# Optimization experiments

Hardware: AMD Instinct MI355X
Metric: run time of the kernel (lower is better)

Reference implementation:

```python
import jax, jax.numpy as jnp
import numpy as np

EPS = 1e-10


def _log_scaling(feats):
    """Raw feats (..., 15): xmin,ymin,xmax,ymax,area,angle,pca_big,pca_small,hu1..hu7
    -> (..., 17): xmin..area, log|pca_big..hu7|, lshape, cosangle, sinangle."""
    lshape = jnp.sqrt(feats[..., 7:8]) / (jnp.sqrt(feats[..., 6:7]) + EPS)
    cosangle = jnp.cos(feats[..., 5:6])
    sinangle = jnp.sin(feats[..., 5:6])
    logged = jnp.log(jnp.abs(feats[..., 5:]) + EPS)  # cols 5..14 logged
    # original drops the (logged) angle column 5 and keeps logged cols 6..14
    return jnp.concatenate([feats[..., :5], logged[..., 1:], lshape, cosangle, sinangle], axis=-1)


def _make_parents(n_trees, P, seed=0):
    """Valid topologically-ordered tree: parent[p] < p, parent[0] = 0 (root)."""
    rng = np.random.default_rng(seed)
    idx = np.arange(P)
    high = np.maximum(idx, 1)
    par = rng.integers(0, 2**31 - 1, size=(n_trees, P)) % high[None, :]
    par[:, 0] = 0
    return par.astype(np.int32)


def setup_inputs() -> dict:
    key = jax.random.key(0)
    k1, k2, k3, k4 = jax.random.split(key, 4)
    B, N, H, W = 2, 2, 1024, 1024
    P = H * W
    x = jax.random.normal(k1, (B, N, H, W), dtype=jnp.float32) * 10.0
    weight = jax.random.uniform(k2, (N, 17, 1), dtype=jnp.float32, minval=-0.01, maxval=0.01)
    bias = jnp.zeros((N, 1), dtype=jnp.float32)
    attrs = jax.random.uniform(k3, (B, N, P, 15), dtype=jnp.float32) * 4.0
    parents = jnp.asarray(_make_parents(B * N, P).reshape(B, N, P))
    return {"x": x, "weight": weight, "bias": bias, "attrs": attrs, "parents": parents}


def _path_sum(contrib_pad, par_pad, P):
    """Pointer-doubling root-to-node path sums over a tree with sentinel at index P."""
    iters = max(int(np.ceil(np.log2(max(P, 2)))), 1)

    def body(i, carry):
        v, p = carry
        return v + v[p], p[p]

    v, _ = jax.lax.fori_loop(0, iters, body, (contrib_pad, par_pad))
    return v[:P]


def reference(x, weight, bias, attrs, parents):
    B, N, H, W = x.shape
    P = H * W
    xf = x.reshape(B, N, P)
    idx = jnp.arange(P, dtype=parents.dtype)
    is_root = parents == idx  # (B,N,P)
    parent_vals = jnp.take_along_axis(xf, parents, axis=-1)
    diff = jnp.where(is_root, xf, xf - parent_vals)  # per-node gray-level increment
    feats = _log_scaling(attrs)  # (B,N,P,17)
    lin = jnp.einsum('bnpf,nfo->bnpo', feats, weight) + bias[None, :, None, :]
    scores = jax.nn.sigmoid(lin[..., 0])  # (B,N,P)
    contrib = diff * scores
    # sentinel node P with contribution 0; roots point at the sentinel
    sent = jnp.full((B, N, 1), P, dtype=parents.dtype)
    par_pad = jnp.concatenate([jnp.where(is_root, P, parents), sent], axis=-1)
    contrib_pad = jnp.concatenate([contrib, jnp.zeros((B, N, 1), x.dtype)], axis=-1)
    out = jax.vmap(jax.vmap(lambda c, p: _path_sum(c, p, P)))(contrib_pad, par_pad)
    return out.reshape(B, N, H, W)
```

## Files before the change

### kernel.cpp

```cpp
#include <hip/hip_runtime.h>
#include <math.h>

#define EPSF 1e-10f
#define P_NODES (1 << 20)
#define T_FRONT 65536
#define T_MID   262144

struct __align__(8) NodePair {
    float v;
    int   par;
};

__global__ __launch_bounds__(256) void score_kernel(
    const float* __restrict__ x,
    const float* __restrict__ weight,
    const float* __restrict__ bias,
    const float* __restrict__ attrs,
    const int*   __restrict__ parents,
    NodePair*    __restrict__ dst,
    int N)
{
    __shared__ float sA[256 * 15];

    const int t = threadIdx.x;
    const int blockBase = blockIdx.x * 256;
    const int idx = blockBase + t;

    const float4* ab4 = (const float4*)(attrs + (size_t)blockBase * 15);
    float4* sA4 = (float4*)sA;
#pragma unroll
    for (int k = t; k < 960; k += 256)
        sA4[k] = ab4[k];

    const int tree = blockBase >> 20;
    const int n    = tree % N;
    const float* w = weight + n * 17;
    const float  b = bias[n];

    __syncthreads();

    const float* a = &sA[t * 15];

    float acc = b;
    acc += a[0] * w[0];
    acc += a[1] * w[1];
    acc += a[2] * w[2];
    acc += a[3] * w[3];
    acc += a[4] * w[4];

    const float a5 = a[5];
    const float a6 = a[6];
    const float a7 = a[7];

    acc += __logf(fabsf(a6)    + EPSF) * w[5];
    acc += __logf(fabsf(a7)    + EPSF) * w[6];
    acc += __logf(fabsf(a[8])  + EPSF) * w[7];
    acc += __logf(fabsf(a[9])  + EPSF) * w[8];
    acc += __logf(fabsf(a[10]) + EPSF) * w[9];
    acc += __logf(fabsf(a[11]) + EPSF) * w[10];
    acc += __logf(fabsf(a[12]) + EPSF) * w[11];
    acc += __logf(fabsf(a[13]) + EPSF) * w[12];
    acc += __logf(fabsf(a[14]) + EPSF) * w[13];

    const float lshape = __fsqrt_rn(a7) / (__fsqrt_rn(a6) + EPSF);
    acc += lshape * w[14];
    acc += __cosf(a5) * w[15];
    acc += __sinf(a5) * w[16];

    const float score = 1.0f / (1.0f + __expf(-acc));

    const int   p   = idx & (P_NODES - 1);
    const int   par = parents[idx];
    const float xv  = x[idx];

    NodePair r;
    if (par == p) {
        r.v   = xv * score;
        r.par = -1;
    } else {
        r.v   = (xv - x[(idx - p) + par]) * score;
        r.par = par;
    }
    dst[idx] = r;
}

__global__ __launch_bounds__(256) void frontier_kernel(
    const NodePair* __restrict__ pairs,
    float*          __restrict__ out)
{
    const int j  = blockIdx.x * blockDim.x + threadIdx.x;
    const int p0 = j * 2;
    if (p0 >= T_FRONT) return;

    const int base = blockIdx.y << 20;
    const NodePair* tp = pairs + base;

    float4 r = *(const float4*)(tp + p0);
    float s0 = r.x;  int c0 = __float_as_int(r.y);
    float s1 = r.z;  int c1 = __float_as_int(r.w);

    while (c0 >= 0 || c1 >= 0) {
        NodePair q0, q1;
        bool a0 = (c0 >= 0), a1 = (c1 >= 0);
        if (a0) q0 = tp[c0];
        if (a1) q1 = tp[c1];
        if (a0) { s0 += q0.v; c0 = q0.par; }
        if (a1) { s1 += q1.v; c1 = q1.par; }
    }

    float2 o; o.x = s0; o.y = s1;
    *(float2*)(out + base + p0) = o;
}

__global__ __launch_bounds__(256) void chunk_kernel(
    const NodePair* __restrict__ pairs,
    float*          __restrict__ out,
    int lo, int hi)
{
    const int j  = blockIdx.x * blockDim.x + threadIdx.x;
    const int p0 = lo + j * 2;
    if (p0 >= hi) return;

    const int base = blockIdx.y << 20;
    const NodePair* tp = pairs + base;

    float4 r = *(const float4*)(tp + p0);
    float s0 = r.x;  int c0 = __float_as_int(r.y);
    float s1 = r.z;  int c1 = __float_as_int(r.w);

    bool a0 = (c0 >= lo), a1 = (c1 >= lo);
    while (a0 || a1) {
        NodePair q0, q1;
        if (a0) q0 = tp[c0];
        if (a1) q1 = tp[c1];
        if (a0) { s0 += q0.v; c0 = q0.par; a0 = (c0 >= lo); }
        if (a1) { s1 += q1.v; c1 = q1.par; a1 = (c1 >= lo); }
    }
    s0 += out[base + c0];
    s1 += out[base + c1];

    float2 o; o.x = s0; o.y = s1;
    *(float2*)(out + base + p0) = o;
}

extern "C" void kernel_launch(void* const* d_in, const int* in_sizes, int n_in,
                              void* d_out, int out_size, void* d_ws, size_t ws_size,
                              hipStream_t stream)
{
    const float* x       = (const float*)d_in[0];
    const float* weight  = (const float*)d_in[1];
    const float* bias    = (const float*)d_in[2];
    const float* attrs   = (const float*)d_in[3];
    const int*   parents = (const int*)d_in[4];
    float*       out     = (float*)d_out;

    const int total  = in_sizes[0];
    const int N      = in_sizes[1] / 17;
    const int nTrees = total >> 20;

    NodePair* pairs = (NodePair*)d_ws;

    const int block = 256;
    const int grid  = (total + block - 1) / block;

    score_kernel<<<grid, block, 0, stream>>>(x, weight, bias, attrs, parents,
                                             pairs, N);

    {
        dim3 g((T_FRONT / 2 + block - 1) / block, nTrees);
        frontier_kernel<<<g, block, 0, stream>>>(pairs, out);
    }
    {
        dim3 g(((T_MID - T_FRONT) / 2 + block - 1) / block, nTrees);
        chunk_kernel<<<g, block, 0, stream>>>(pairs, out, T_FRONT, T_MID);
    }
    {
        dim3 g(((P_NODES - T_MID) / 2 + block - 1) / block, nTrees);
        chunk_kernel<<<g, block, 0, stream>>>(pairs, out, T_MID, P_NODES);
    }
}
```

Measured before the change: 440.6 us.

## Interleave tree blocks across XCDs, add chunk stage, nontemporal loads/stores

Remaps block indices so consecutive blocks alternate between trees in pairs, aiming for better cache locality per XCD. Splits the chunked path-sum into three stages instead of two, which shortens the walks done in the last stage at the cost of one more launch. The frontier kernel now handles one node per thread instead of two. Adds nontemporal loads for attrs and nontemporal stores for the final output to reduce cache pollution. The block remap hardcodes 4 trees and assumes sizes divide evenly.

```diff
diff --git a/kernel.cpp b/kernel.cpp
--- a/kernel.cpp
+++ b/kernel.cpp
@@ -4,12 +4,22 @@
 #define EPSF 1e-10f
 #define P_NODES (1 << 20)
 #define T_FRONT 65536
-#define T_MID   262144
+#define T_C1    262144
+#define T_C2    524288
+
+typedef float vf4 __attribute__((ext_vector_type(4)));
+typedef float vf2 __attribute__((ext_vector_type(2)));
 
 struct __align__(8) NodePair {
     float v;
     int   par;
 };
+
+__device__ __forceinline__ void tree_decomp(int b, int& tree, int& jj)
+{
+    tree = (b & 7) >> 1;
+    jj   = ((b >> 3) << 1) | (b & 1);
+}
 
 __global__ __launch_bounds__(256) void score_kernel(
     const float* __restrict__ x,
@@ -23,16 +33,17 @@
     __shared__ float sA[256 * 15];
 
     const int t = threadIdx.x;
-    const int blockBase = blockIdx.x * 256;
+    int tree, jj;
+    tree_decomp(blockIdx.x, tree, jj);
+    const int blockBase = (tree << 20) + (jj << 8);
     const int idx = blockBase + t;
 
-    const float4* ab4 = (const float4*)(attrs + (size_t)blockBase * 15);
-    float4* sA4 = (float4*)sA;
+    const vf4* ab4 = (const vf4*)(attrs + (size_t)blockBase * 15);
+    vf4* sA4 = (vf4*)sA;
 #pragma unroll
     for (int k = t; k < 960; k += 256)
-        sA4[k] = ab4[k];
+        sA4[k] = __builtin_nontemporal_load(&ab4[k]);
 
-    const int tree = blockBase >> 20;
     const int n    = tree % N;
     const float* w = weight + n * 17;
     const float  b = bias[n];
@@ -88,40 +99,32 @@
     const NodePair* __restrict__ pairs,
     float*          __restrict__ out)
 {
-    const int j  = blockIdx.x * blockDim.x + threadIdx.x;
-    const int p0 = j * 2;
-    if (p0 >= T_FRONT) return;
-
-    const int base = blockIdx.y << 20;
+    int tree, jj;
+    tree_decomp(blockIdx.x, tree, jj);
+    const int p    = (jj << 8) + threadIdx.x;
+    const int base = tree << 20;
     const NodePair* tp = pairs + base;
 
-    float4 r = *(const float4*)(tp + p0);
-    float s0 = r.x;  int c0 = __float_as_int(r.y);
-    float s1 = r.z;  int c1 = __float_as_int(r.w);
-
-    while (c0 >= 0 || c1 >= 0) {
-        NodePair q0, q1;
-        bool a0 = (c0 >= 0), a1 = (c1 >= 0);
-        if (a0) q0 = tp[c0];
-        if (a1) q1 = tp[c1];
-        if (a0) { s0 += q0.v; c0 = q0.par; }
-        if (a1) { s1 += q1.v; c1 = q1.par; }
+    NodePair r = tp[p];
+    float s = r.v;
+    int   c = r.par;
+    while (c >= 0) {
+        NodePair q = tp[c];
+        s += q.v;
+        c  = q.par;
     }
-
-    float2 o; o.x = s0; o.y = s1;
-    *(float2*)(out + base + p0) = o;
+    out[base + p] = s;
 }
 
 __global__ __launch_bounds__(256) void chunk_kernel(
     const NodePair* __restrict__ pairs,
     float*          __restrict__ out,
-    int lo, int hi)
+    int lo, int last)
 {
-    const int j  = blockIdx.x * blockDim.x + threadIdx.x;
-    const int p0 = lo + j * 2;
-    if (p0 >= hi) return;
-
-    const int base = blockIdx.y << 20;
+    int tree, jj;
+    tree_decomp(blockIdx.x, tree, jj);
+    const int p0   = lo + ((((jj << 8) + threadIdx.x)) << 1);
+    const int base = tree << 20;
     const NodePair* tp = pairs + base;
 
     float4 r = *(const float4*)(tp + p0);
@@ -139,8 +142,11 @@
     s0 += out[base + c0];
     s1 += out[base + c1];
 
-    float2 o; o.x = s0; o.y = s1;
-    *(float2*)(out + base + p0) = o;
+    vf2 o; o.x = s0; o.y = s1;
+    if (last)
+        __builtin_nontemporal_store(o, (vf2*)(out + base + p0));
+    else
+        *(vf2*)(out + base + p0) = o;
 }
 
 extern "C" void kernel_launch(void* const* d_in, const int* in_sizes, int n_in,
@@ -161,21 +167,18 @@
     NodePair* pairs = (NodePair*)d_ws;
 
     const int block = 256;
-    const int grid  = (total + block - 1) / block;
 
-    score_kernel<<<grid, block, 0, stream>>>(x, weight, bias, attrs, parents,
-                                             pairs, N);
+    score_kernel<<<total / block, block, 0, stream>>>(x, weight, bias, attrs,
+                                                      parents, pairs, N);
 
-    {
-        dim3 g((T_FRONT / 2 + block - 1) / block, nTrees);
-        frontier_kernel<<<g, block, 0, stream>>>(pairs, out);
-    }
-    {
-        dim3 g(((T_MID - T_FRONT) / 2 + block - 1) / block, nTrees);
-        chunk_kernel<<<g, block, 0, stream>>>(pairs, out, T_FRONT, T_MID);
-    }
-    {
-        dim3 g(((P_NODES - T_MID) / 2 + block - 1) / block, nTrees);
-        chunk_kernel<<<g, block, 0, stream>>>(pairs, out, T_MID, P_NODES);
-    }
+    frontier_kernel<<<(T_FRONT / block) * nTrees, block, 0, stream>>>(pairs, out);
+
+    chunk_kernel<<<((T_C1 - T_FRONT) / (2 * block)) * nTrees, block, 0, stream>>>(
+        pairs, out, T_FRONT, 0);
+
+    chunk_kernel<<<((T_C2 - T_C1) / (2 * block)) * nTrees, block, 0, stream>>>(
+        pairs, out, T_C1, 0);
+
+    chunk_kernel<<<((P_NODES - T_C2) / (2 * block)) * nTrees, block, 0, stream>>>(
+        pairs, out, T_C2, 1);
 }
```

Result: faster. 401.2 us (-8.9%).
